# Kernel optimization log

Measured on AMD Instinct MI355X. Metric: run time of the kernel, lower is better.

Reference implementation:

```python
import jax, jax.numpy as jnp
import numpy as np
from jax import lax

B, C_IN, H, W = 32, 128, 64, 64
K, C_OUT, KS = 8, 128, 3
HID = C_IN * 4  # extend = 4
TEMPERATURE = 1.0
PAD = 1


def setup_inputs() -> dict:
    key = jax.random.key(0)
    ks = jax.random.split(key, 7)
    x = jax.random.normal(ks[0], (B, C_IN, H, W), jnp.float32)
    prompt_param = jax.random.uniform(ks[1], (1, K, HID), jnp.float32)
    w1 = jax.random.normal(ks[2], (HID, C_IN), jnp.float32) * 0.05
    b1 = jnp.zeros((HID,), jnp.float32)
    w2 = jax.random.normal(ks[3], (HID, HID), jnp.float32) * 0.05
    b2 = jnp.zeros((HID,), jnp.float32)
    kernels_weights = jax.random.normal(ks[4], (K, C_OUT, C_IN, KS, KS), jnp.float32) * 0.05
    kernels_bias = jax.random.normal(ks[5], (K, C_OUT), jnp.float32) * 0.05
    return {
        'x': x, 'prompt_param': prompt_param,
        'w1': w1, 'b1': b1, 'w2': w2, 'b2': b2,
        'kernels_weights': kernels_weights, 'kernels_bias': kernels_bias,
    }


def reference(x, prompt_param, w1, b1, w2, b2, kernels_weights, kernels_bias):
    # Attention: global avg pool -> MLP -> prompt dot -> softmax over kernels
    pooled = jnp.mean(x, axis=(2, 3))                       # (B, C_in)
    h = jax.nn.relu(pooled @ w1.T + b1)                     # (B, HID)
    s = h @ w2.T + b2                                       # (B, HID)
    scores = jnp.sum(s[:, None, :] * prompt_param, axis=-1)  # (B, K)
    alphas = jax.nn.softmax(scores / TEMPERATURE, axis=-1)   # (B, K)

    # Per-sample kernel aggregation
    agg_w = jnp.einsum('bk,koihw->boihw', alphas, kernels_weights)  # (B,O,I,kh,kw)
    agg_b = alphas @ kernels_bias                                    # (B, O)

    # Per-sample conv2d (equivalent to the groups=B grouped-conv trick)
    def conv_one(xi, wi):
        # xi: (C_in,H,W), wi: (O,C_in,kh,kw)
        return lax.conv_general_dilated(
            xi[None], wi, window_strides=(1, 1),
            padding=((PAD, PAD), (PAD, PAD)),
            dimension_numbers=('NCHW', 'OIHW', 'NCHW'))[0]
    out = jax.vmap(conv_one)(x, agg_w)                       # (B,O,H,W)
    out = out + agg_b[:, :, None, None]
    return out
```

## Files before the change

### kernel.cpp

```cpp
#include <hip/hip_runtime.h>
#include <hip/hip_bf16.h>
#include <stdint.h>


typedef __bf16 v8bf __attribute__((ext_vector_type(8)));
typedef float  v4f  __attribute__((ext_vector_type(4)));

#define XT_OFF     0u
#define XT_BYTES   (32u*4096u*128u*2u)
#define AGGW_OFF   (XT_OFF + XT_BYTES)
#define AGGW_BYTES (32u*9u*128u*128u*2u)
#define PART_OFF   (AGGW_OFF)
#define POOLED_OFF (AGGW_OFF + 0x100000u)
#define H_OFF      (AGGW_OFF + 0x110000u)
#define PSCORE_OFF (AGGW_OFF + 0x120000u)
#define ALPHA_OFF  (AGGW_OFF + AGGW_BYTES)
#define ALPHA_BYTES (32u*8u*4u)
#define AGGB_OFF   (ALPHA_OFF + ALPHA_BYTES)
#define AGGB_BYTES (32u*128u*4u)

typedef const void __attribute__((address_space(1))) gconst_t;
typedef void       __attribute__((address_space(3))) ldsv_t;

__device__ __forceinline__ void g2l16(const void* g, void* l) {
  __builtin_amdgcn_global_load_lds((gconst_t*)g, (ldsv_t*)l, 16, 0, 0);
}

__global__ __launch_bounds__(256) void pool_convert_kernel(
    const float* __restrict__ x, float* __restrict__ partial,
    __hip_bfloat16* __restrict__ xT) {
  const int b = blockIdx.x >> 6;
  const int h = blockIdx.x & 63;
  const int tid = threadIdx.x;
  const int wv = tid >> 6, lane = tid & 63;
  __shared__ __align__(16) __hip_bfloat16 sT[64 * 130];

  const float* xrow = x + (((size_t)b * 128) << 12) + (h << 6);
  for (int i = 0; i < 32; ++i) {
    int c = wv * 32 + i;
    float v = xrow[((size_t)c << 12) + lane];
    sT[lane * 130 + c] = __float2bfloat16(v);
    float s = v;
    #pragma unroll
    for (int m = 32; m > 0; m >>= 1) s += __shfl_xor(s, m);
    if (lane == 0) partial[((b << 6) + h) * 128 + c] = s;
  }
  __syncthreads();
  const int pw = tid >> 2;
  const int piece = tid & 3;
  const uint32_t* s32 = (const uint32_t*)sT;
  uint32_t vals[16];
  #pragma unroll
  for (int j = 0; j < 16; ++j) vals[j] = s32[pw * 65 + piece * 16 + j];
  char* dst = (char*)xT + ((((size_t)b << 6) + h) * 64 + pw) * 256 + piece * 64;
  #pragma unroll
  for (int j = 0; j < 4; ++j)
    ((uint4*)dst)[j] = make_uint4(vals[4*j], vals[4*j+1], vals[4*j+2], vals[4*j+3]);
}

__global__ __launch_bounds__(128) void pool_reduce_kernel(
    const float* __restrict__ partial, float* __restrict__ pooled) {
  const int b = blockIdx.x, c = threadIdx.x;
  float acc = 0.0f;
  const float* src = partial + ((size_t)b << 6) * 128 + c;
  #pragma unroll 8
  for (int h = 0; h < 64; ++h) acc += src[h * 128];
  pooled[b * 128 + c] = acc * (1.0f / 4096.0f);
}

__global__ __launch_bounds__(256) void attn_l1_kernel(
    const float* __restrict__ pooled, const float* __restrict__ w1,
    const float* __restrict__ b1, float* __restrict__ hbuf) {
  const int jt = blockIdx.x * 8;
  const int tid = threadIdx.x;
  __shared__ float sW[8 * 132];
  __shared__ float sPool[32 * 132];

  {
    int r = tid >> 5, c4 = (tid & 31) * 4;
    *(float4*)&sW[r * 132 + c4] = *(const float4*)&w1[(jt + r) * 128 + c4];
  }
  #pragma unroll
  for (int q = 0; q < 4; ++q) {
    int idx = q * 256 + tid;
    int bb = idx >> 5, c4 = (idx & 31) * 4;
    *(float4*)&sPool[bb * 132 + c4] = *(const float4*)&pooled[bb * 128 + c4];
  }
  __syncthreads();

  const int b = tid >> 3, jr = tid & 7;
  float acc = 0.0f;
  #pragma unroll
  for (int i4 = 0; i4 < 32; ++i4) {
    float4 pv = *(const float4*)&sPool[b * 132 + i4 * 4];
    float4 wv = *(const float4*)&sW[jr * 132 + i4 * 4];
    acc += pv.x * wv.x + pv.y * wv.y + pv.z * wv.z + pv.w * wv.w;
  }
  hbuf[b * 512 + jt + jr] = fmaxf(acc + b1[jt + jr], 0.0f);
}

__global__ __launch_bounds__(256) void attn_l2s_kernel(
    const float* __restrict__ hbuf, const float* __restrict__ w2,
    const float* __restrict__ b2, const float* __restrict__ prompt,
    float* __restrict__ pscore) {
  const int jtile = blockIdx.x >> 1;
  const int bg = blockIdx.x & 1;
  const int jt = jtile * 8;
  const int tid = threadIdx.x;
  __shared__ float sW2[8 * 516];
  __shared__ float sH[16 * 516];
  __shared__ float sSc[16 * 9];
  __shared__ float sPr[64];

  #pragma unroll
  for (int q = 0; q < 4; ++q) {
    int idx = q * 256 + tid;
    int r = idx >> 7, c4 = (idx & 127) * 4;
    *(float4*)&sW2[r * 516 + c4] = *(const float4*)&w2[(jt + r) * 512 + c4];
  }
  #pragma unroll
  for (int q = 0; q < 8; ++q) {
    int idx = q * 256 + tid;
    int r = idx >> 7, c4 = (idx & 127) * 4;
    *(float4*)&sH[r * 516 + c4] =
        *(const float4*)&hbuf[(bg * 16 + r) * 512 + c4];
  }
  if (tid < 64) sPr[tid] = prompt[(tid >> 3) * 512 + jt + (tid & 7)];
  __syncthreads();

  const int pair = tid >> 1, half = tid & 1;
  const int bl = pair >> 3, jr = pair & 7;
  float acc = 0.0f;
  #pragma unroll
  for (int i4 = 0; i4 < 64; ++i4) {
    int idx = (half * 64 + i4) * 4;
    float4 hv = *(const float4*)&sH[bl * 516 + idx];
    float4 wv = *(const float4*)&sW2[jr * 516 + idx];
    acc += hv.x * wv.x + hv.y * wv.y + hv.z * wv.z + hv.w * wv.w;
  }
  acc += __shfl_xor(acc, 1);
  if (half == 0) sSc[bl * 9 + jr] = acc + b2[jt + jr];
  __syncthreads();

  if (tid < 128) {
    int bl = tid >> 3, k = tid & 7;
    float p = 0.0f;
    #pragma unroll
    for (int jj = 0; jj < 8; ++jj) p = fmaf(sSc[bl * 9 + jj], sPr[k * 8 + jj], p);
    pscore[((size_t)(jtile * 32 + bg * 16 + bl)) * 8 + k] = p;
  }
}

__global__ __launch_bounds__(256) void softmax_aggb_kernel(
    const float* __restrict__ pscore, const float* __restrict__ kbias,
    float* __restrict__ alphas, float* __restrict__ aggb) {
  const int b = blockIdx.x;
  const int tid = threadIdx.x;
  __shared__ float sRed[32 * 8], sSc[8], sA[8];

  {
    int jt2 = tid >> 3, k = tid & 7;
    sRed[jt2 * 8 + k] = pscore[((size_t)(jt2 * 32 + b)) * 8 + k] +
                        pscore[((size_t)((jt2 + 32) * 32 + b)) * 8 + k];
  }
  __syncthreads();
  if (tid < 8) {
    float sc = 0.0f;
    #pragma unroll
    for (int j = 0; j < 32; ++j) sc += sRed[j * 8 + tid];
    sSc[tid] = sc;
  }
  __syncthreads();
  if (tid == 0) {
    float mx = sSc[0];
    for (int k = 1; k < 8; ++k) mx = fmaxf(mx, sSc[k]);
    float sum = 0.0f, e[8];
    for (int k = 0; k < 8; ++k) { e[k] = expf(sSc[k] - mx); sum += e[k]; }
    float inv = 1.0f / sum;
    for (int k = 0; k < 8; ++k) sA[k] = e[k] * inv;
  }
  __syncthreads();
  if (tid < 8) alphas[b * 8 + tid] = sA[tid];
  if (tid < 128) {
    float acc = 0.0f;
    #pragma unroll
    for (int k = 0; k < 8; ++k) acc = fmaf(sA[k], kbias[k * 128 + tid], acc);
    aggb[b * 128 + tid] = acc;
  }
}

__global__ __launch_bounds__(128) void agg_weights_kernel(
    const float* __restrict__ kw, const float* __restrict__ alphas,
    __hip_bfloat16* __restrict__ aggw) {
  const int co = blockIdx.x;
  const int bg = blockIdx.y;
  const int tid = threadIdx.x;
  __shared__ float sA[64];
  __shared__ float sbuf[1152];
  if (tid < 64) sA[tid] = alphas[bg * 64 + tid];
  __syncthreads();

  float acc[8][9];
  #pragma unroll
  for (int bb = 0; bb < 8; ++bb)
    #pragma unroll
    for (int q = 0; q < 9; ++q) acc[bb][q] = 0.0f;

  for (int k = 0; k < 8; ++k) {
    const float* src = kw + ((size_t)(k * 128 + co)) * 1152;
    float v[9];
    #pragma unroll
    for (int q = 0; q < 9; ++q) v[q] = src[tid + 128 * q];
    #pragma unroll
    for (int bb = 0; bb < 8; ++bb) {
      float a = sA[bb * 8 + k];
      #pragma unroll
      for (int q = 0; q < 9; ++q) acc[bb][q] = fmaf(a, v[q], acc[bb][q]);
    }
  }

  #pragma unroll 1
  for (int bb = 0; bb < 8; ++bb) {
    __syncthreads();
    #pragma unroll
    for (int q = 0; q < 9; ++q) sbuf[tid + 128 * q] = acc[bb][q];
    __syncthreads();
    const int b = bg * 8 + bb;
    #pragma unroll
    for (int t = 0; t < 9; ++t)
      aggw[(((size_t)(b * 9 + t) * 128 + co) << 7) + tid] =
          __float2bfloat16(sbuf[tid * 9 + t]);
  }
}

#define XTILE_B 33792
#define ATILE_B 8192

__global__ __launch_bounds__(256) void dyn_conv_kernel(
    const __hip_bfloat16* __restrict__ xT, const __hip_bfloat16* __restrict__ aggw,
    const float* __restrict__ aggb, float* __restrict__ out) {
  const int tile = blockIdx.x;
  const int b    = blockIdx.y;
  const int tid  = threadIdx.x;
  const int wv = tid >> 6, lane = tid & 63;
  const int wm = wv >> 1, wn = wv & 1;
  const int lm = lane & 15, quad = lane >> 4;
  const int r0 = tile * 2;

  __shared__ __align__(16) char smem[XTILE_B + 2 * ATILE_B + 512];
  char* xb = smem;
  char* abuf = smem + XTILE_B;
  float* sBias = (float*)(smem + XTILE_B + 2 * ATILE_B);

  if (tid < 128) sBias[tid] = aggb[b * 128 + tid];

  for (int pos = tid; pos < 264; pos += 256) {
    int tr = pos / 66, tc = pos - tr * 66;
    int h = r0 - 1 + tr, w = tc - 1;
    if ((unsigned)h >= 64u || (unsigned)w >= 64u) {
      int4* d = (int4*)(xb + pos * 128);
      #pragma unroll
      for (int i = 0; i < 8; ++i) d[i] = make_int4(0, 0, 0, 0);
    }
  }

  const char* xTb = (const char*)xT + ((size_t)b << 20);
  const char* awb = (const char*)aggw + (size_t)b * 294912;

  auto stageX = [&](int half) {
    for (int i = wv; i < 33; i += 4) {
      int P = (i << 6) + lane;
      int pos = P >> 3, slot = P & 7;
      int tr = pos / 66, tc = pos - tr * 66;
      int h = r0 - 1 + tr, w = tc - 1;
      char* dst = xb + (i << 10);
      if ((unsigned)h < 64u && (unsigned)w < 64u) {
        int p = slot ^ (pos & 7);
        const char* src = xTb + (((h << 6) + w) << 8) + (half << 7) + (p << 4);
        g2l16(src, dst);
      }
    }
  };
  auto stageA = [&](int c) {
    int tap = (c % 18) >> 1;
    int cic = ((c / 18) << 1) | (c & 1);
    char* ab = abuf + (c & 1) * ATILE_B;
    const char* base = awb + (tap << 15);
    #pragma unroll
    for (int jj = 0; jj < 2; ++jj) {
      int j = wv * 2 + jj;
      int co = (j << 4) + (lane >> 2);
      int f = lane & 3;
      int p = f ^ ((co >> 1) & 3);
      const char* src = base + (co << 8) + (cic << 6) + (p << 4);
      g2l16(src, ab + (j << 10));
    }
  };

  int posb[4];
  #pragma unroll
  for (int ni = 0; ni < 4; ++ni) {
    int n = wn * 64 + ni * 16 + lm;
    posb[ni] = (n >> 6) * 66 + (n & 63);
  }
  const int fA = (quad ^ ((lm >> 1) & 3)) << 4;
  int aoff[4];
  #pragma unroll
  for (int mi = 0; mi < 4; ++mi) {
    int co = wm * 64 + mi * 16 + lm;
    aoff[mi] = (co << 6) + fA;
  }

  v4f acc[4][4];
  #pragma unroll
  for (int mi = 0; mi < 4; ++mi)
    #pragma unroll
    for (int ni = 0; ni < 4; ++ni) acc[mi][ni] = v4f{0.f, 0.f, 0.f, 0.f};

  auto computeChunk = [&](int c) {
    int tap = (c % 18) >> 1, sub = c & 1;
    int th = tap / 3, tw = tap - th * 3;
    char* ab = abuf + (c & 1) * ATILE_B;
    v8bf af[4], bfr[4];
    #pragma unroll
    for (int mi = 0; mi < 4; ++mi) af[mi] = *(const v8bf*)(ab + aoff[mi]);
    const int piece = (sub << 2) | quad;
    #pragma unroll
    for (int ni = 0; ni < 4; ++ni) {
      int pos = posb[ni] + th * 66 + tw;
      int pp = (piece ^ (pos & 7)) << 4;
      bfr[ni] = *(const v8bf*)(xb + (pos << 7) + pp);
    }
    #pragma unroll
    for (int mi = 0; mi < 4; ++mi)
      #pragma unroll
      for (int ni = 0; ni < 4; ++ni)
        acc[mi][ni] = __builtin_amdgcn_mfma_f32_16x16x32_bf16(
            af[mi], bfr[ni], acc[mi][ni], 0, 0, 0);
  };

  stageX(0);
  stageA(0);
  __syncthreads();
  for (int c = 0; c < 18; ++c) {
    if (c < 17) stageA(c + 1);
    computeChunk(c);
    __syncthreads();
  }
  stageX(1);
  stageA(18);
  __syncthreads();
  for (int c = 18; c < 36; ++c) {
    if (c < 35) stageA(c + 1);
    computeChunk(c);
    __syncthreads();
  }

  #pragma unroll
  for (int mi = 0; mi < 4; ++mi) {
    #pragma unroll
    for (int r = 0; r < 4; ++r) {
      int co = wm * 64 + mi * 16 + quad * 4 + r;
      float bias = sBias[co];
      #pragma unroll
      for (int ni = 0; ni < 4; ++ni) {
        int n = wn * 64 + ni * 16 + lm;
        out[(((size_t)(b * 128 + co)) << 12) + tile * 128 + n] =
            acc[mi][ni][r] + bias;
      }
    }
  }
}

extern "C" void kernel_launch(void* const* d_in, const int* in_sizes, int n_in,
                              void* d_out, int out_size, void* d_ws, size_t ws_size,
                              hipStream_t stream) {
  const float* x      = (const float*)d_in[0];
  const float* prompt = (const float*)d_in[1];
  const float* w1     = (const float*)d_in[2];
  const float* b1     = (const float*)d_in[3];
  const float* w2     = (const float*)d_in[4];
  const float* b2     = (const float*)d_in[5];
  const float* kw     = (const float*)d_in[6];
  const float* kb     = (const float*)d_in[7];
  float* out = (float*)d_out;
  char* ws = (char*)d_ws;

  __hip_bfloat16* xT   = (__hip_bfloat16*)(ws + XT_OFF);
  __hip_bfloat16* aggw = (__hip_bfloat16*)(ws + AGGW_OFF);
  float* part   = (float*)(ws + PART_OFF);
  float* pooled = (float*)(ws + POOLED_OFF);
  float* hbuf   = (float*)(ws + H_OFF);
  float* pscore = (float*)(ws + PSCORE_OFF);
  float* alphas = (float*)(ws + ALPHA_OFF);
  float* aggb   = (float*)(ws + AGGB_OFF);

  pool_convert_kernel<<<2048, 256, 0, stream>>>(x, part, xT);
  pool_reduce_kernel<<<32, 128, 0, stream>>>(part, pooled);
  attn_l1_kernel<<<64, 256, 0, stream>>>(pooled, w1, b1, hbuf);
  attn_l2s_kernel<<<128, 256, 0, stream>>>(hbuf, w2, b2, prompt, pscore);
  softmax_aggb_kernel<<<32, 256, 0, stream>>>(pscore, kb, alphas, aggb);
  agg_weights_kernel<<<dim3(128, 4), 128, 0, stream>>>(kw, alphas, aggw);
  dyn_conv_kernel<<<dim3(32, 32), 256, 0, stream>>>(xT, aggw, aggb, out);
}
```

Baseline: 230.2 us.

## Load aggregated weight fragments directly from global memory instead of LDS staging

Removes the double-buffered LDS staging of the per-sample weight tiles and the per-chunk __syncthreads. Each wave now reads its A fragments straight from global memory (through cache) inside fully unrolled chunk loops, which shrinks shared memory and may allow more blocks per CU. In exchange, weight loads are no longer shared across waves through LDS. The A reads also become redundant across the two waves that share a row block, and global latency is exposed unless the compiler hoists the loads.

```diff
diff --git a/kernel.cpp b/kernel.cpp
--- a/kernel.cpp
+++ b/kernel.cpp
@@ -234,7 +234,6 @@
 }
 
 #define XTILE_B 33792
-#define ATILE_B 8192
 
 __global__ __launch_bounds__(256) void dyn_conv_kernel(
     const __hip_bfloat16* __restrict__ xT, const __hip_bfloat16* __restrict__ aggw,
@@ -247,10 +246,9 @@
   const int lm = lane & 15, quad = lane >> 4;
   const int r0 = tile * 2;
 
-  __shared__ __align__(16) char smem[XTILE_B + 2 * ATILE_B + 512];
+  __shared__ __align__(16) char smem[XTILE_B + 512];
   char* xb = smem;
-  char* abuf = smem + XTILE_B;
-  float* sBias = (float*)(smem + XTILE_B + 2 * ATILE_B);
+  float* sBias = (float*)(smem + XTILE_B);
 
   if (tid < 128) sBias[tid] = aggb[b * 128 + tid];
 
@@ -281,21 +279,6 @@
       }
     }
   };
-  auto stageA = [&](int c) {
-    int tap = (c % 18) >> 1;
-    int cic = ((c / 18) << 1) | (c & 1);
-    char* ab = abuf + (c & 1) * ATILE_B;
-    const char* base = awb + (tap << 15);
-    #pragma unroll
-    for (int jj = 0; jj < 2; ++jj) {
-      int j = wv * 2 + jj;
-      int co = (j << 4) + (lane >> 2);
-      int f = lane & 3;
-      int p = f ^ ((co >> 1) & 3);
-      const char* src = base + (co << 8) + (cic << 6) + (p << 4);
-      g2l16(src, ab + (j << 10));
-    }
-  };
 
   int posb[4];
   #pragma unroll
@@ -303,12 +286,11 @@
     int n = wn * 64 + ni * 16 + lm;
     posb[ni] = (n >> 6) * 66 + (n & 63);
   }
-  const int fA = (quad ^ ((lm >> 1) & 3)) << 4;
-  int aoff[4];
+  const char* aBase[4];
   #pragma unroll
   for (int mi = 0; mi < 4; ++mi) {
     int co = wm * 64 + mi * 16 + lm;
-    aoff[mi] = (co << 6) + fA;
+    aBase[mi] = awb + (co << 8) + (quad << 4);
   }
 
   v4f acc[4][4];
@@ -317,13 +299,14 @@
     #pragma unroll
     for (int ni = 0; ni < 4; ++ni) acc[mi][ni] = v4f{0.f, 0.f, 0.f, 0.f};
 
-  auto computeChunk = [&](int c) {
-    int tap = (c % 18) >> 1, sub = c & 1;
-    int th = tap / 3, tw = tap - th * 3;
-    char* ab = abuf + (c & 1) * ATILE_B;
+  auto computeChunk = [&](int half, int c) {
+    const int tap = c >> 1, sub = c & 1;
+    const int th = tap / 3, tw = tap - th * 3;
+    const int cic = (half << 1) | sub;
     v8bf af[4], bfr[4];
     #pragma unroll
-    for (int mi = 0; mi < 4; ++mi) af[mi] = *(const v8bf*)(ab + aoff[mi]);
+    for (int mi = 0; mi < 4; ++mi)
+      af[mi] = *(const v8bf*)(aBase[mi] + (tap << 15) + (cic << 6));
     const int piece = (sub << 2) | quad;
     #pragma unroll
     for (int ni = 0; ni < 4; ++ni) {
@@ -340,21 +323,14 @@
   };
 
   stageX(0);
-  stageA(0);
-  __syncthreads();
-  for (int c = 0; c < 18; ++c) {
-    if (c < 17) stageA(c + 1);
-    computeChunk(c);
-    __syncthreads();
-  }
+  __syncthreads();
+  #pragma unroll
+  for (int c = 0; c < 18; ++c) computeChunk(0, c);
+  __syncthreads();
   stageX(1);
-  stageA(18);
-  __syncthreads();
-  for (int c = 18; c < 36; ++c) {
-    if (c < 35) stageA(c + 1);
-    computeChunk(c);
-    __syncthreads();
-  }
+  __syncthreads();
+  #pragma unroll
+  for (int c = 0; c < 18; ++c) computeChunk(1, c);
 
   #pragma unroll
   for (int mi = 0; mi < 4; ++mi) {
```

Measured after the change: 261.0 us. 1.13x slower.
